# Kernel optimization log

Measured on AMD Instinct MI355X. Metric: run time of the kernel, lower is better.

The kernel has to match this reference:

```python
import jax, jax.numpy as jnp
import numpy as np

B, S, D = 64, 4096, 1024

def setup_inputs() -> dict:
    key = jax.random.key(0)
    k1, k2, k3 = jax.random.split(key, 3)
    inp = jax.random.normal(k1, (B, S, D), dtype=jnp.float32)
    lens = jax.random.randint(k2, (B,), 1, S + 1, dtype=jnp.int32)  # lengths in [1, S]
    w = jax.random.normal(k3, (1, D), dtype=jnp.float32) * (1.0 / np.sqrt(D))
    b = jnp.zeros((1,), dtype=jnp.float32)
    return {"inp": inp, "lens": lens, "w": w, "b": b}

def reference(inp, lens, w, b):
    # scores[b,s] = inp[b,s,:] @ w[0,:] + b
    scores = jnp.einsum("bsd,d->bs", inp, w[0]) + b[0]            # [B, S]
    mask = jnp.arange(inp.shape[1])[None, :] < lens[:, None]       # [B, S]
    scores = jnp.where(mask, scores, -jnp.inf)
    attn = jax.nn.softmax(scores, axis=1)                          # [B, S]
    context = jnp.einsum("bs,bsd->bd", attn, inp)                  # [B, D]
    return context
```

## Files before the change

kernel.cpp:

```cpp
#include <hip/hip_runtime.h>
#include <math.h>

#define BATCH 64
#define SEQ   4096
#define DIM   1024

__global__ __launch_bounds__(256)
void attn_partial_kernel(const float* __restrict__ inp,
                         const int*   __restrict__ lens,
                         const float* __restrict__ w,
                         float* __restrict__ ws_c,
                         float* __restrict__ ws_m,
                         float* __restrict__ ws_l,
                         int splits, int chunk)
{
    const int split = blockIdx.x;
    const int b     = blockIdx.y;
    const int t     = threadIdx.x;
    const int wave  = t >> 6;
    const int lane  = t & 63;
    const int colb  = lane * 4;

    __shared__ float c_s[4][DIM];
    __shared__ float m_s[4];
    __shared__ float l_s[4];

    const int len = lens[b];
    const int s0  = split * chunk;
    const int s1  = min(s0 + chunk, len);

    const float4 w0 = *(const float4*)(w       + colb);
    const float4 w1 = *(const float4*)(w + 256 + colb);
    const float4 w2 = *(const float4*)(w + 512 + colb);
    const float4 w3 = *(const float4*)(w + 768 + colb);

    float  m  = -INFINITY, l = 0.0f;
    float4 c0 = {0,0,0,0}, c1 = {0,0,0,0}, c2 = {0,0,0,0}, c3 = {0,0,0,0};

    const float* base = inp + (size_t)b * SEQ * DIM + colb;

    for (int s = s0 + wave; s < s1; s += 4) {
        const float* rp = base + (size_t)s * DIM;
        const float4 x0 = *(const float4*)(rp);
        const float4 x1 = *(const float4*)(rp + 256);
        const float4 x2 = *(const float4*)(rp + 512);
        const float4 x3 = *(const float4*)(rp + 768);

        float pd = x0.x*w0.x + x0.y*w0.y + x0.z*w0.z + x0.w*w0.w
                 + x1.x*w1.x + x1.y*w1.y + x1.z*w1.z + x1.w*w1.w
                 + x2.x*w2.x + x2.y*w2.y + x2.z*w2.z + x2.w*w2.w
                 + x3.x*w3.x + x3.y*w3.y + x3.z*w3.z + x3.w*w3.w;

        #pragma unroll
        for (int off = 32; off > 0; off >>= 1)
            pd += __shfl_xor(pd, off, 64);

        const float mn    = fmaxf(m, pd);
        const float alpha = __expf(m - mn);
        const float p     = __expf(pd - mn);
        l = l * alpha + p;
        c0.x = c0.x*alpha + p*x0.x;  c0.y = c0.y*alpha + p*x0.y;
        c0.z = c0.z*alpha + p*x0.z;  c0.w = c0.w*alpha + p*x0.w;
        c1.x = c1.x*alpha + p*x1.x;  c1.y = c1.y*alpha + p*x1.y;
        c1.z = c1.z*alpha + p*x1.z;  c1.w = c1.w*alpha + p*x1.w;
        c2.x = c2.x*alpha + p*x2.x;  c2.y = c2.y*alpha + p*x2.y;
        c2.z = c2.z*alpha + p*x2.z;  c2.w = c2.w*alpha + p*x2.w;
        c3.x = c3.x*alpha + p*x3.x;  c3.y = c3.y*alpha + p*x3.y;
        c3.z = c3.z*alpha + p*x3.z;  c3.w = c3.w*alpha + p*x3.w;
        m = mn;
    }

    *(float4*)&c_s[wave][colb      ] = c0;
    *(float4*)&c_s[wave][colb + 256] = c1;
    *(float4*)&c_s[wave][colb + 512] = c2;
    *(float4*)&c_s[wave][colb + 768] = c3;
    if (lane == 0) { m_s[wave] = m; l_s[wave] = l; }
    __syncthreads();

    const float M = fmaxf(fmaxf(m_s[0], m_s[1]), fmaxf(m_s[2], m_s[3]));
    float sc[4];
    float L = 0.0f;
    #pragma unroll
    for (int iw = 0; iw < 4; ++iw) {
        sc[iw] = (m_s[iw] == -INFINITY) ? 0.0f : __expf(m_s[iw] - M);
        L += sc[iw] * l_s[iw];
    }

    const int oc = t * 4;
    float4 acc = {0,0,0,0};
    #pragma unroll
    for (int iw = 0; iw < 4; ++iw) {
        const float4 ci = *(const float4*)&c_s[iw][oc];
        acc.x += sc[iw]*ci.x; acc.y += sc[iw]*ci.y;
        acc.z += sc[iw]*ci.z; acc.w += sc[iw]*ci.w;
    }

    const size_t idx = (size_t)b * splits + split;
    *(float4*)(ws_c + idx * DIM + oc) = acc;
    if (t == 0) { ws_m[idx] = M; ws_l[idx] = L; }
}

__global__ __launch_bounds__(256)
void attn_reduce_kernel(const float* __restrict__ ws_c,
                        const float* __restrict__ ws_m,
                        const float* __restrict__ ws_l,
                        float* __restrict__ out, int splits)
{
    const int b  = blockIdx.x;
    const int t  = threadIdx.x;
    const int oc = t * 4;

    const float* mb = ws_m + (size_t)b * splits;
    const float* lb = ws_l + (size_t)b * splits;

    float M = -INFINITY;
    for (int i = 0; i < splits; ++i) M = fmaxf(M, mb[i]);

    float  L   = 0.0f;
    float4 acc = {0,0,0,0};
    for (int i = 0; i < splits; ++i) {
        const float mi  = mb[i];
        const float scl = (mi == -INFINITY) ? 0.0f : __expf(mi - M);
        L += scl * lb[i];
        const float4 ci = *(const float4*)(ws_c + ((size_t)b * splits + i) * DIM + oc);
        acc.x += scl*ci.x; acc.y += scl*ci.y;
        acc.z += scl*ci.z; acc.w += scl*ci.w;
    }
    const float inv = 1.0f / L;
    float4 o = { acc.x*inv, acc.y*inv, acc.z*inv, acc.w*inv };
    *(float4*)(out + (size_t)b * DIM + oc) = o;
}

extern "C" void kernel_launch(void* const* d_in, const int* in_sizes, int n_in,
                              void* d_out, int out_size, void* d_ws, size_t ws_size,
                              hipStream_t stream) {
    const float* inp  = (const float*)d_in[0];
    const int*   lens = (const int*)  d_in[1];
    const float* w    = (const float*)d_in[2];
    float* out = (float*)d_out;

    int splits = 32;
    while (splits > 1 &&
           (size_t)BATCH * splits * (DIM + 2) * sizeof(float) > ws_size)
        splits >>= 1;
    const int chunk = SEQ / splits;

    float* wsf  = (float*)d_ws;
    float* ws_c = wsf;
    float* ws_m = wsf + (size_t)BATCH * splits * DIM;
    float* ws_l = ws_m + (size_t)BATCH * splits;

    attn_partial_kernel<<<dim3(splits, BATCH), 256, 0, stream>>>(
        inp, lens, w, ws_c, ws_m, ws_l, splits, chunk);
    attn_reduce_kernel<<<BATCH, 256, 0, stream>>>(ws_c, ws_m, ws_l, out, splits);
}
```

Measured before the change: 1.261 ms.

## Balance split chunks by sequence length and unroll row loop by four

Derives each block's chunk size from the batch's actual length so all splits get equal valid rows, and gives each wave a contiguous subrange. Processes four rows per iteration with sixteen outstanding vector loads and a combined online-softmax update to raise memory-level parallelism. Adds an occupancy hint and unroll pragmas in the reduce kernel. Higher register use may reduce occupancy.

```diff
diff --git a/kernel.cpp b/kernel.cpp
--- a/kernel.cpp
+++ b/kernel.cpp
@@ -5,14 +5,14 @@
 #define SEQ   4096
 #define DIM   1024
 
-__global__ __launch_bounds__(256)
+__global__ __launch_bounds__(256, 4)
 void attn_partial_kernel(const float* __restrict__ inp,
                          const int*   __restrict__ lens,
                          const float* __restrict__ w,
                          float* __restrict__ ws_c,
                          float* __restrict__ ws_m,
                          float* __restrict__ ws_l,
-                         int splits, int chunk)
+                         int splits)
 {
     const int split = blockIdx.x;
     const int b     = blockIdx.y;
@@ -25,21 +25,71 @@
     __shared__ float m_s[4];
     __shared__ float l_s[4];
 
-    const int len = lens[b];
-    const int s0  = split * chunk;
-    const int s1  = min(s0 + chunk, len);
+    const int len   = lens[b];
+    const int chunk = (len + splits - 1) / splits;
+    const int s0    = split * chunk;
+    const int s1    = min(s0 + chunk, len);
+    const int n     = max(s1 - s0, 0);
+    const int per   = (n + 3) >> 2;
+    const int ws0   = s0 + wave * per;
+    const int ws1   = min(ws0 + per, s1);
 
     const float4 w0 = *(const float4*)(w       + colb);
     const float4 w1 = *(const float4*)(w + 256 + colb);
     const float4 w2 = *(const float4*)(w + 512 + colb);
     const float4 w3 = *(const float4*)(w + 768 + colb);
 
-    float  m  = -INFINITY, l = 0.0f;
+    float  m = -INFINITY, l = 0.0f;
     float4 c0 = {0,0,0,0}, c1 = {0,0,0,0}, c2 = {0,0,0,0}, c3 = {0,0,0,0};
 
     const float* base = inp + (size_t)b * SEQ * DIM + colb;
 
-    for (int s = s0 + wave; s < s1; s += 4) {
+    int s = ws0;
+    for (; s + 4 <= ws1; s += 4) {
+        const float* rp = base + (size_t)s * DIM;
+        float4 x[4][4];
+        #pragma unroll
+        for (int j = 0; j < 4; ++j)
+            #pragma unroll
+            for (int q = 0; q < 4; ++q)
+                x[j][q] = *(const float4*)(rp + j * DIM + q * 256);
+
+        float pd[4];
+        #pragma unroll
+        for (int j = 0; j < 4; ++j) {
+            const float4 a0 = x[j][0], a1 = x[j][1], a2 = x[j][2], a3 = x[j][3];
+            pd[j] = a0.x*w0.x + a0.y*w0.y + a0.z*w0.z + a0.w*w0.w
+                  + a1.x*w1.x + a1.y*w1.y + a1.z*w1.z + a1.w*w1.w
+                  + a2.x*w2.x + a2.y*w2.y + a2.z*w2.z + a2.w*w2.w
+                  + a3.x*w3.x + a3.y*w3.y + a3.z*w3.z + a3.w*w3.w;
+        }
+
+        #pragma unroll
+        for (int off = 32; off > 0; off >>= 1) {
+            #pragma unroll
+            for (int j = 0; j < 4; ++j)
+                pd[j] += __shfl_xor(pd[j], off, 64);
+        }
+
+        const float mn = fmaxf(m, fmaxf(fmaxf(pd[0], pd[1]), fmaxf(pd[2], pd[3])));
+        const float alpha = __expf(m - mn);
+        float p[4];
+        #pragma unroll
+        for (int j = 0; j < 4; ++j) p[j] = __expf(pd[j] - mn);
+        l = l * alpha + p[0] + p[1] + p[2] + p[3];
+
+        #pragma unroll
+        for (int q = 0; q < 4; ++q) {
+            float4* cq = (q == 0) ? &c0 : (q == 1) ? &c1 : (q == 2) ? &c2 : &c3;
+            cq->x = cq->x*alpha + p[0]*x[0][q].x + p[1]*x[1][q].x + p[2]*x[2][q].x + p[3]*x[3][q].x;
+            cq->y = cq->y*alpha + p[0]*x[0][q].y + p[1]*x[1][q].y + p[2]*x[2][q].y + p[3]*x[3][q].y;
+            cq->z = cq->z*alpha + p[0]*x[0][q].z + p[1]*x[1][q].z + p[2]*x[2][q].z + p[3]*x[3][q].z;
+            cq->w = cq->w*alpha + p[0]*x[0][q].w + p[1]*x[1][q].w + p[2]*x[2][q].w + p[3]*x[3][q].w;
+        }
+        m = mn;
+    }
+
+    for (; s < ws1; ++s) {
         const float* rp = base + (size_t)s * DIM;
         const float4 x0 = *(const float4*)(rp);
         const float4 x1 = *(const float4*)(rp + 256);
@@ -50,7 +100,6 @@
                  + x1.x*w1.x + x1.y*w1.y + x1.z*w1.z + x1.w*w1.w
                  + x2.x*w2.x + x2.y*w2.y + x2.z*w2.z + x2.w*w2.w
                  + x3.x*w3.x + x3.y*w3.y + x3.z*w3.z + x3.w*w3.w;
-
         #pragma unroll
         for (int off = 32; off > 0; off >>= 1)
             pd += __shfl_xor(pd, off, 64);
@@ -114,10 +163,12 @@
     const float* lb = ws_l + (size_t)b * splits;
 
     float M = -INFINITY;
+    #pragma unroll 8
     for (int i = 0; i < splits; ++i) M = fmaxf(M, mb[i]);
 
     float  L   = 0.0f;
     float4 acc = {0,0,0,0};
+    #pragma unroll 4
     for (int i = 0; i < splits; ++i) {
         const float mi  = mb[i];
         const float scl = (mi == -INFINITY) ? 0.0f : __expf(mi - M);
@@ -143,7 +194,6 @@
     while (splits > 1 &&
            (size_t)BATCH * splits * (DIM + 2) * sizeof(float) > ws_size)
         splits >>= 1;
-    const int chunk = SEQ / splits;
 
     float* wsf  = (float*)d_ws;
     float* ws_c = wsf;
@@ -151,6 +201,6 @@
     float* ws_l = ws_m + (size_t)BATCH * splits;
 
     attn_partial_kernel<<<dim3(splits, BATCH), 256, 0, stream>>>(
-        inp, lens, w, ws_c, ws_m, ws_l, splits, chunk);
+        inp, lens, w, ws_c, ws_m, ws_l, splits);
     attn_reduce_kernel<<<BATCH, 256, 0, stream>>>(ws_c, ws_m, ws_l, out, splits);
 }
```

Result: no change. 1.246 ms (-1.2%).
